# Optimization experiments

Measured on AMD Instinct MI355X. Metric: run time of the kernel, lower is better.

Reference implementation:

```python
import math
import jax, jax.numpy as jnp
import numpy as np

B, S, D, H, L, V = 2, 1024, 1024, 16, 6, 256
HD = D // H  # 64
PAD = 0


def setup_inputs() -> dict:
    key = jax.random.key(0)
    ks = jax.random.split(key, 22)
    s = 0.02
    f32 = jnp.float32
    inp = {
        "x": jax.random.randint(ks[0], (B, S), 0, V, dtype=jnp.int32),
        "emb": (jax.random.normal(ks[1], (V, D)) * s).astype(f32),
        "Wq": (jax.random.normal(ks[2], (L, D, D)) * s).astype(f32),
        "bq": jnp.zeros((L, D), f32),
        "Wk": (jax.random.normal(ks[3], (L, D, D)) * s).astype(f32),
        "bk": jnp.zeros((L, D), f32),
        "Wv": (jax.random.normal(ks[4], (L, D, D)) * s).astype(f32),
        "bv": jnp.zeros((L, D), f32),
        "Wo": (jax.random.normal(ks[5], (L, D, D)) * s).astype(f32),
        "bo": jnp.zeros((L, D), f32),
        "W1": (jax.random.normal(ks[6], (L, D, D // 2)) * s).astype(f32),
        "b1": jnp.zeros((L, D // 2), f32),
        "W2": (jax.random.normal(ks[7], (L, D // 2, D)) * s).astype(f32),
        "b2": jnp.zeros((L, D), f32),
        "g1": jnp.ones((L, D), f32),
        "be1": jnp.zeros((L, D), f32),
        "g2": jnp.ones((L, D), f32),
        "be2": jnp.zeros((L, D), f32),
        "E": jax.random.normal(ks[8], (L, S, HD)).astype(f32),  # relative pos embeddings, non-trainable
        "Wf": (jax.random.normal(ks[9], (D, V)) * s).astype(f32),
        "bf": jnp.zeros((V,), f32),
    }
    return inp


def _layernorm(x, g, b, eps=1e-6):
    mu = jnp.mean(x, axis=-1, keepdims=True)
    var = jnp.mean((x - mu) ** 2, axis=-1, keepdims=True)
    return (x - mu) * jax.lax.rsqrt(var + eps) * g + b


def _pos_encoding():
    # embed[p, i] = sin(p * exp(-ln(1e4)*i/D) * exp(ln(1e4)*(i%2)/D) + 0.5*pi*(i%2))
    i = jnp.arange(D, dtype=jnp.float32)
    par = jnp.mod(i, 2.0)
    rate = jnp.exp(-math.log(10000.0) * i / D) * jnp.exp(math.log(10000.0) * par / D)
    pos = jnp.arange(S, dtype=jnp.float32)
    return jnp.sin(pos[:, None] * rate[None, :] + 0.5 * math.pi * par[None, :])  # [S, D]


def _skew(QE):
    # Music Transformer skewing: pad one col on the left, reshape, drop first row.
    padded = jnp.pad(QE, ((0, 0), (0, 0), (0, 0), (1, 0)))  # [B,H,S,S+1]
    reshaped = padded.reshape(B, H, S + 1, S)
    return reshaped[:, :, 1:, :]  # [B,H,S,S]


def reference(x, emb, Wq, bq, Wk, bk, Wv, bv, Wo, bo, W1, b1, W2, b2,
              g1, be1, g2, be2, E, Wf, bf):
    pe = _pos_encoding()
    # look-ahead mask: pad positions OR strictly-future positions
    pad_mask = (x == PAD)[:, None, None, :]                      # [B,1,1,S]
    causal = jnp.triu(jnp.ones((S, S), bool), k=1)[None, None]   # [1,1,S,S]
    neg = (pad_mask | causal).astype(jnp.float32) * -1e9         # [B,1,S,S]
    # QE mask: keep qe[i, j] only where j >= S-1-i (upper-right triangle)
    idx = jnp.arange(S)
    qe_mask = (idx[None, :] >= (S - 1 - idx)[:, None]).astype(jnp.float32)

    h = emb[x] * math.sqrt(D) + pe[None]  # [B,S,D]
    scale = 1.0 / math.sqrt(HD)
    for l in range(L):
        q = (h @ Wq[l] + bq[l]).reshape(B, S, H, HD).transpose(0, 2, 1, 3)
        k = (h @ Wk[l] + bk[l]).reshape(B, S, H, HD).transpose(0, 2, 1, 3)
        v = (h @ Wv[l] + bv[l]).reshape(B, S, H, HD).transpose(0, 2, 1, 3)
        QE = jnp.einsum('bhld,md->bhlm', q, E[l]) * qe_mask
        Srel = _skew(QE)
        logits = (jnp.einsum('bhld,bhmd->bhlm', q, k) + Srel) * scale + neg
        aw = jax.nn.softmax(logits, axis=-1)
        attn = jnp.einsum('bhlm,bhmd->bhld', aw, v)
        attn = attn.transpose(0, 2, 1, 3).reshape(B, S, D)
        ao = attn @ Wo[l] + bo[l]
        o1 = _layernorm(ao, g1[l], be1[l])          # NOTE: no residual, as in source
        f = jax.nn.relu(o1 @ W1[l] + b1[l]) @ W2[l] + b2[l]
        h = _layernorm(f, g2[l], be2[l])
    return h @ Wf + bf  # [B,S,V]
```

## Files before the change

### kernel.cpp

```cpp
#include <hip/hip_runtime.h>
#include <hip/hip_bf16.h>


typedef __attribute__((ext_vector_type(8))) short  s8_t;
typedef __attribute__((ext_vector_type(4))) short  s4_t;
typedef __attribute__((ext_vector_type(8))) __bf16 bf8_t;
typedef __attribute__((ext_vector_type(4))) float  f4v;

static __device__ __forceinline__ short f2bf(float f) {
  union { float f; unsigned u; } a; a.f = f;
  unsigned u = a.u;
  u += 0x7fffu + ((u >> 16) & 1u);
  return (short)(u >> 16);
}
static __device__ __forceinline__ float bf2f(short s) {
  union { float f; unsigned u; } a;
  a.u = ((unsigned)(unsigned short)s) << 16;
  return a.f;
}
static __device__ __forceinline__ f4v mfma16(s8_t a, s8_t b, f4v c) {
  return __builtin_amdgcn_mfma_f32_16x16x32_bf16(
      __builtin_bit_cast(bf8_t, a), __builtin_bit_cast(bf8_t, b), c, 0, 0, 0);
}
static __device__ __forceinline__ void gld16(const short* g, short* l) {
  __builtin_amdgcn_global_load_lds(
      (const __attribute__((address_space(1))) void*)g,
      (__attribute__((address_space(3))) void*)l, 16, 0, 0);
}

static __device__ const int IT_TAB[40] = {
  15,15,15,15, 14,14,14,14, 13,13,13,13, 12,12,12,12,
  11,11,11, 10,10,10, 9,9,9, 8,8,8,
  7,7, 6,6, 5,5, 4,4, 3, 2, 1, 0};
static __device__ const int CW_TAB[40] = {
  0,1,2,3, 0,1,2,3, 0,1,2,3, 0,1,2,3,
  0,1,2, 0,1,2, 0,1,2, 0,1,2,
  0,1, 0,1, 0,1, 0,1, 0, 0, 0, 0};

__global__ void prep_weights(
    const float* __restrict__ Wq, const float* __restrict__ Wk,
    const float* __restrict__ Wv, const float* __restrict__ Wo,
    const float* __restrict__ W1, const float* __restrict__ W2,
    const float* __restrict__ Wf,
    short* __restrict__ qkvT, short* __restrict__ WoT, short* __restrict__ W1T,
    short* __restrict__ W2T, short* __restrict__ WfT) {
  __shared__ float tile[32][33];
  int z = blockIdx.x;
  const float* in; short* out; int R, C; long outBS; int rowOff = 0;
  if (z < 18432) {
    R = 1024; C = 1024; outBS = (long)3072 * 1024; out = qkvT;
    if (z < 6144)       { in = Wq; }
    else if (z < 12288) { in = Wk; rowOff = 1024; z -= 6144; }
    else                { in = Wv; rowOff = 2048; z -= 12288; }
  } else if (z < 24576) { in = Wo; out = WoT; R = 1024; C = 1024; outBS = (long)1024 * 1024; z -= 18432; }
  else if (z < 27648)   { in = W1; out = W1T; R = 1024; C = 512;  outBS = (long)512 * 1024;  z -= 24576; }
  else if (z < 30720)   { in = W2; out = W2T; R = 512;  C = 1024; outBS = (long)1024 * 512;  z -= 27648; }
  else                  { in = Wf; out = WfT; R = 1024; C = 256;  outBS = 0;                 z -= 30720; }
  const int nx = C >> 5, ny = R >> 5;
  const int per = nx * ny;
  const int l = z / per, rem = z % per;
  const int cx = rem % nx, cy = rem / nx;
  in += (long)l * R * C;
  out += (long)l * outBS + (long)rowOff * R;
  const int c0 = cx * 32, r0 = cy * 32;
  const int tx = threadIdx.x, ty = threadIdx.y;
#pragma unroll
  for (int i = 0; i < 4; i++)
    tile[ty + i * 8][tx] = in[(long)(r0 + ty + i * 8) * C + c0 + tx];
  __syncthreads();
#pragma unroll
  for (int i = 0; i < 4; i++)
    out[(long)(c0 + ty + i * 8) * R + r0 + tx] = f2bf(tile[tx][ty + i * 8]);
}

__global__ __launch_bounds__(256) void prep_misc(
    const int* __restrict__ x, const float* __restrict__ emb,
    const float* __restrict__ E,
    const float* __restrict__ bq, const float* __restrict__ bk,
    const float* __restrict__ bv,
    short* __restrict__ h, short* __restrict__ Ebf,
    float* __restrict__ qkvB, int* __restrict__ fnp) {
  const int z = blockIdx.x;
  const int tid = threadIdx.x;
  if (z < 2048) {
    const int s = z & 1023;
    const int xv = x[z];
    const int c = tid << 2;
    const float4 e = *(const float4*)(emb + (long)xv * 1024 + c);
    const float ev[4] = {e.x, e.y, e.z, e.w};
    s4_t o;
#pragma unroll
    for (int i = 0; i < 4; i++) {
      const int d = c + i;
      const float par = (float)(d & 1);
      const float rate = expf(-9.210340371976184f * (float)d / 1024.0f) *
                         expf(9.210340371976184f * par / 1024.0f);
      const float pe = sinf((float)s * rate + 1.5707963267948966f * par);
      o[i] = f2bf(ev[i] * 32.0f + pe);
    }
    *(s4_t*)(h + (long)z * 1024 + c) = o;
  } else if (z < 2432) {
    const long i = ((long)(z - 2048) * 256 + tid) * 4;
    const float4 t = *(const float4*)(E + i);
    s4_t o = {f2bf(t.x), f2bf(t.y), f2bf(t.z), f2bf(t.w)};
    *(s4_t*)(Ebf + i) = o;
  } else if (z < 2504) {
    const int idx = (z - 2432) * 256 + tid;
    const int l = idx / 3072, n = idx % 3072;
    float v = (n < 1024) ? bq[l * 1024 + n]
            : (n < 2048) ? bk[l * 1024 + n - 1024]
                         : bv[l * 1024 + n - 2048];
    qkvB[idx] = v;
  } else {
    if (tid < 64) {
      const int b = z - 2504;
      int first = 1024;
      for (int j0 = 0; j0 < 1024; j0 += 64) {
        unsigned long long m = __ballot(x[b * 1024 + j0 + tid] != 0);
        if (m) { first = j0 + __ffsll(m) - 1; break; }
      }
      if (tid == 0) fnp[b] = first;
    }
  }
}

__global__ __launch_bounds__(256) void ln_kernel(const short* __restrict__ in,
                                                 short* __restrict__ out,
                                                 const float* __restrict__ g,
                                                 const float* __restrict__ be) {
  __shared__ float red[4];
  __shared__ float red2[4];
  const int row = blockIdx.x;
  const int tid = threadIdx.x;
  const int c = tid << 2;
  const s4_t xv = *(const s4_t*)(in + (long)row * 1024 + c);
  const float x0 = bf2f(xv[0]), x1 = bf2f(xv[1]), x2 = bf2f(xv[2]), x3 = bf2f(xv[3]);
  float s = x0 + x1 + x2 + x3;
#pragma unroll
  for (int off = 1; off < 64; off <<= 1) s += __shfl_xor(s, off);
  const int wave = tid >> 6, lane = tid & 63;
  if (lane == 0) red[wave] = s;
  __syncthreads();
  const float mu = (red[0] + red[1] + red[2] + red[3]) * (1.0f / 1024.0f);
  const float d0 = x0 - mu, d1 = x1 - mu, d2 = x2 - mu, d3 = x3 - mu;
  float q = d0 * d0 + d1 * d1 + d2 * d2 + d3 * d3;
#pragma unroll
  for (int off = 1; off < 64; off <<= 1) q += __shfl_xor(q, off);
  if (lane == 0) red2[wave] = q;
  __syncthreads();
  const float var = (red2[0] + red2[1] + red2[2] + red2[3]) * (1.0f / 1024.0f);
  const float rs = rsqrtf(var + 1e-6f);
  const float4 gv = *(const float4*)(g + c);
  const float4 bv = *(const float4*)(be + c);
  s4_t o = {f2bf(d0 * rs * gv.x + bv.x), f2bf(d1 * rs * gv.y + bv.y),
            f2bf(d2 * rs * gv.z + bv.z), f2bf(d3 * rs * gv.w + bv.w)};
  *(s4_t*)(out + (long)row * 1024 + c) = o;
}

template <int BM, int BN, int WR, int WC, int OUT_BF16, int RELU>
__global__ __launch_bounds__(256) void gemm_lds(
    const short* __restrict__ A, const short* __restrict__ BT,
    void* __restrict__ Cv, const float* __restrict__ biasp,
    int K, int lda, int ldb, int ldc) {
  constexpr int AR = BM / 64, BR = BN / 64;
  constexpr int FI = BM / WR / 16, FJ = BN / WC / 16;
  __shared__ short As[BM * 32];
  __shared__ short Bs[BN * 32];
  const int bm = blockIdx.y * BM, bn = blockIdx.x * BN;
  const int tid = threadIdx.x;
  const int wave = tid >> 6, lane = tid & 63;
  const int quad = lane >> 4, l16 = lane & 15;
  const int wr = wave / WC, wc = wave % WC;
  const int wm = wr * (BM / WR), wn = wc * (BN / WC);

  const short* Ag = A + (long)(bm + wave * 16 + (lane >> 2)) * lda + ((lane & 3) << 3);
  const short* Bg = BT + (long)(bn + wave * 16 + (lane >> 2)) * ldb + ((lane & 3) << 3);

  f4v acc[FI][FJ];
#pragma unroll
  for (int i = 0; i < FI; i++)
#pragma unroll
    for (int j = 0; j < FJ; j++) {
      f4v zz = {0.f, 0.f, 0.f, 0.f};
      acc[i][j] = zz;
    }

  for (int k0 = 0; k0 < K; k0 += 32) {
#pragma unroll
    for (int r = 0; r < AR; r++)
      gld16(Ag + (long)r * 64 * lda + k0, As + r * 2048 + wave * 512);
#pragma unroll
    for (int r = 0; r < BR; r++)
      gld16(Bg + (long)r * 64 * ldb + k0, Bs + r * 2048 + wave * 512);
    __syncthreads();
    s8_t af[FI], bfr[FJ];
#pragma unroll
    for (int t = 0; t < FI; t++)
      af[t] = *(const s8_t*)&As[(wm + t * 16 + l16) * 32 + quad * 8];
#pragma unroll
    for (int t = 0; t < FJ; t++)
      bfr[t] = *(const s8_t*)&Bs[(wn + t * 16 + l16) * 32 + quad * 8];
#pragma unroll
    for (int ti = 0; ti < FI; ti++)
#pragma unroll
      for (int tj = 0; tj < FJ; tj++)
        acc[ti][tj] = mfma16(af[ti], bfr[tj], acc[ti][tj]);
    __syncthreads();
  }

#pragma unroll
  for (int ti = 0; ti < FI; ti++) {
#pragma unroll
    for (int tj = 0; tj < FJ; tj++) {
      const int n = bn + wn + tj * 16 + l16;
      const float bval = biasp ? biasp[n] : 0.f;
#pragma unroll
      for (int r = 0; r < 4; r++) {
        const int m = bm + wm + ti * 16 + quad * 4 + r;
        float vv = acc[ti][tj][r] + bval;
        if (RELU) vv = fmaxf(vv, 0.f);
        if (OUT_BF16) ((short*)Cv)[(long)m * ldc + n] = f2bf(vv);
        else          ((float*)Cv)[(long)m * ldc + n] = vv;
      }
    }
  }
}

__global__ __launch_bounds__(256) void attn_main(
    const short* __restrict__ qkv, const short* __restrict__ Eb,
    const int* __restrict__ xids, const int* __restrict__ fnp,
    float* __restrict__ PO, float* __restrict__ PM, float* __restrict__ PL,
    short* __restrict__ outb) {
  __shared__ short Ks2[8][128][8];
  __shared__ short Vt[64][136];
  __shared__ short Gs[4][16][152];
  __shared__ float kneg[128];

  const int bh = blockIdx.x, b = bh >> 4, hh = bh & 15;
  const int yy = blockIdx.y;
  const bool fbp = (yy >= 40);
  const int itile = fbp ? (yy - 40) : IT_TAB[yy];
  const int cw = fbp ? 0 : CW_TAB[yy];
  const int fb = fnp[b];
  const int i0g = itile * 64;
  if (fbp && fb <= i0g) return;

  const int tid = threadIdx.x;
  const int wave = tid >> 6, lane = tid & 63, quad = lane >> 4, l16 = lane & 15;
  const int i0 = i0g + wave * 16;

  s8_t aq[2];
  {
    const short* qp = qkv + ((long)(b * 1024 + i0 + l16)) * 3072 + hh * 64 + quad * 8;
    aq[0] = *(const s8_t*)qp;
    aq[1] = *(const s8_t*)(qp + 32);
  }

  f4v o[4];
#pragma unroll
  for (int nt = 0; nt < 4; nt++) { f4v zz = {0.f, 0.f, 0.f, 0.f}; o[nt] = zz; }
  float m_run[4] = {-INFINITY, -INFINITY, -INFINITY, -INFINITY};
  float l_run[4] = {0.f, 0.f, 0.f, 0.f};

  const int half = wave >> 1;
  const int krow = ((wave & 1) << 6) + lane;
  const short* kbase = qkv + (long)b * 1024 * 3072 + 1024 + hh * 64 + wave * 8;
  const short* vbase = qkv + (long)b * 1024 * 3072 + 2048 + hh * 64 + half * 32;
  short* gs = &Gs[wave][0][0];

  const int jBeg = fbp ? 0 : cw * 256;
  const int jEnd = fbp ? 1024 : min(cw * 256 + 256, i0g + 64);

  for (int j0 = jBeg; j0 < jEnd; j0 += 128) {
    {
      const long k1 = min(j0 + lane, 1023);
      const long k2 = min(j0 + 64 + lane, 1023);
      gld16(kbase + k1 * 3072, &Ks2[wave][0][0]);
      gld16(kbase + k2 * 3072, &Ks2[wave][64][0]);
      gld16(kbase + k1 * 3072 + 32, &Ks2[wave + 4][0][0]);
      gld16(kbase + k2 * 3072 + 32, &Ks2[wave + 4][64][0]);
      const long kv = min(j0 + krow, 1023);
      const short* vrow = vbase + kv * 3072;
      const s8_t v0 = *(const s8_t*)(vrow);
      const s8_t v1 = *(const s8_t*)(vrow + 8);
      const s8_t v2 = *(const s8_t*)(vrow + 16);
      const s8_t v3 = *(const s8_t*)(vrow + 24);
#pragma unroll
      for (int t = 0; t < 8; t++) {
        Vt[half * 32 + t][krow] = v0[t];
        Vt[half * 32 + 8 + t][krow] = v1[t];
        Vt[half * 32 + 16 + t][krow] = v2[t];
        Vt[half * 32 + 24 + t][krow] = v3[t];
      }
    }
    if (tid < 128) kneg[tid] = (xids[b * 1024 + min(j0 + tid, 1023)] == 0) ? -1e9f : 0.0f;

    {
      const int mW = 1008 - i0g - wave * 16 + j0;
#pragma unroll
      for (int t = 0; t < 9; t++) {
        const int m = min(mW + t * 16 + l16, 1023);
        const short* ep = Eb + m * 64 + quad * 8;
        const s8_t eb0 = *(const s8_t*)ep;
        const s8_t eb1 = *(const s8_t*)(ep + 32);
        f4v g = {0.f, 0.f, 0.f, 0.f};
        g = mfma16(aq[0], eb0, g);
        g = mfma16(aq[1], eb1, g);
#pragma unroll
        for (int r = 0; r < 4; r++)
          gs[(quad * 4 + r) * 152 + t * 16 + l16] = f2bf(g[r]);
      }
    }
    __syncthreads();

    float p[8][4];
    const int irow = i0 + quad * 4;
#pragma unroll
    for (int jt = 0; jt < 8; jt++) {
      const s8_t k0f = *(const s8_t*)&Ks2[quad][jt * 16 + l16][0];
      const s8_t k1f = *(const s8_t*)&Ks2[4 + quad][jt * 16 + l16][0];
      f4v zz = {0.f, 0.f, 0.f, 0.f};
      zz = mfma16(aq[0], k0f, zz);
      zz = mfma16(aq[1], k1f, zz);
      const int j = j0 + jt * 16 + l16;
      const float kn = kneg[jt * 16 + l16];
#pragma unroll
      for (int r = 0; r < 4; r++) {
        const int rr = quad * 4 + r;
        const float smv = bf2f(gs[rr * 151 + 15 + jt * 16 + l16]);
        const bool causal = (j <= irow + r);
        const float srel = causal ? smv : 0.f;
        const float kk = fbp ? 0.f : (causal ? kn : -1e9f);
        p[jt][r] = (zz[r] + srel) * 0.125f + kk;
      }
    }

    float alpha[4];
#pragma unroll
    for (int r = 0; r < 4; r++) {
      float mx = p[0][r];
#pragma unroll
      for (int jt = 1; jt < 8; jt++) mx = fmaxf(mx, p[jt][r]);
      mx = fmaxf(mx, __shfl_xor(mx, 1));
      mx = fmaxf(mx, __shfl_xor(mx, 2));
      mx = fmaxf(mx, __shfl_xor(mx, 4));
      mx = fmaxf(mx, __shfl_xor(mx, 8));
      const float mnew = fmaxf(m_run[r], mx);
      alpha[r] = expf(m_run[r] - mnew);
      float ps = 0.f;
#pragma unroll
      for (int jt = 0; jt < 8; jt++) {
        p[jt][r] = expf(p[jt][r] - mnew);
        ps += p[jt][r];
      }
      ps += __shfl_xor(ps, 1);
      ps += __shfl_xor(ps, 2);
      ps += __shfl_xor(ps, 4);
      ps += __shfl_xor(ps, 8);
      l_run[r] = l_run[r] * alpha[r] + ps;
      m_run[r] = mnew;
    }

#pragma unroll
    for (int jt = 0; jt < 8; jt++)
#pragma unroll
      for (int r = 0; r < 4; r++)
        gs[(quad * 4 + r) * 152 + jt * 16 + l16] = f2bf(p[jt][r]);
#pragma unroll
    for (int nt = 0; nt < 4; nt++)
#pragma unroll
      for (int r = 0; r < 4; r++)
        o[nt][r] *= alpha[r];

#pragma unroll
    for (int ks4 = 0; ks4 < 4; ks4++) {
      const s8_t ap = *(const s8_t*)&gs[l16 * 152 + ks4 * 32 + quad * 8];
#pragma unroll
      for (int nt = 0; nt < 4; nt++) {
        const s8_t vf = *(const s8_t*)&Vt[nt * 16 + l16][ks4 * 32 + quad * 8];
        o[nt] = mfma16(ap, vf, o[nt]);
      }
    }
    __syncthreads();
  }

  if (fbp) {
#pragma unroll
    for (int nt = 0; nt < 4; nt++)
#pragma unroll
      for (int r = 0; r < 4; r++) {
        const int i = i0 + quad * 4 + r;
        if (i < fb)
          outb[((long)(b * 1024 + i)) * 1024 + hh * 64 + nt * 16 + l16] =
              f2bf(o[nt][r] / l_run[r]);
      }
  } else if (yy >= 36) {
#pragma unroll
    for (int nt = 0; nt < 4; nt++)
#pragma unroll
      for (int r = 0; r < 4; r++) {
        const int i = i0 + quad * 4 + r;
        if (i >= fb)
          outb[((long)(b * 1024 + i)) * 1024 + hh * 64 + nt * 16 + l16] =
              f2bf(o[nt][r] / l_run[r]);
      }
  } else {
    const long part = (long)(bh * 16 + itile) * 4 + cw;
    float* po = PO + part * 4096;
#pragma unroll
    for (int nt = 0; nt < 4; nt++)
#pragma unroll
      for (int r = 0; r < 4; r++) {
        const int row = wave * 16 + quad * 4 + r;
        po[row * 64 + nt * 16 + l16] = o[nt][r];
      }
    if (l16 == 0) {
#pragma unroll
      for (int r = 0; r < 4; r++) {
        const int row = wave * 16 + quad * 4 + r;
        PM[part * 64 + row] = m_run[r];
        PL[part * 64 + row] = l_run[r];
      }
    }
  }
}

__global__ __launch_bounds__(256) void attn_combine(
    const float* __restrict__ PO, const float* __restrict__ PM,
    const float* __restrict__ PL, const int* __restrict__ fnp,
    short* __restrict__ outb) {
  const int id = blockIdx.x;
  const int bh = id / 12, itile = 4 + id % 12;
  const int b = bh >> 4, hh = bh & 15;
  const int nc = (itile >> 2) + 1;
  const int row = threadIdx.x >> 2, seg = (threadIdx.x & 3) << 4;
  const long base = (long)(bh * 16 + itile) * 4;
  const int i = itile * 64 + row;
  if (i < fnp[b]) return;

  float mv[4];
  float M = -INFINITY;
  for (int c = 0; c < nc; c++) {
    mv[c] = PM[(base + c) * 64 + row];
    M = fmaxf(M, mv[c]);
  }
  f4v acc[4];
#pragma unroll
  for (int t = 0; t < 4; t++) { f4v zz = {0.f, 0.f, 0.f, 0.f}; acc[t] = zz; }
  float l = 0.f;
  for (int c = 0; c < nc; c++) {
    const float w = expf(mv[c] - M);
    l += w * PL[(base + c) * 64 + row];
    const float* po = PO + (base + c) * 4096 + row * 64 + seg;
#pragma unroll
    for (int t = 0; t < 4; t++) {
      const f4v v = *(const f4v*)(po + t * 4);
      acc[t] += w * v;
    }
  }
  const float inv = 1.0f / l;
  short* op = outb + ((long)(b * 1024 + i)) * 1024 + hh * 64 + seg;
#pragma unroll
  for (int t = 0; t < 4; t++) {
    s4_t o = {f2bf(acc[t][0] * inv), f2bf(acc[t][1] * inv),
              f2bf(acc[t][2] * inv), f2bf(acc[t][3] * inv)};
    *(s4_t*)(op + t * 4) = o;
  }
}

extern "C" void kernel_launch(void* const* d_in, const int* in_sizes, int n_in,
                              void* d_out, int out_size, void* d_ws, size_t ws_size,
                              hipStream_t stream) {
  const int*   x   = (const int*)d_in[0];
  const float* emb = (const float*)d_in[1];
  const float* Wq  = (const float*)d_in[2];
  const float* bq  = (const float*)d_in[3];
  const float* Wk  = (const float*)d_in[4];
  const float* bk  = (const float*)d_in[5];
  const float* Wv  = (const float*)d_in[6];
  const float* bv  = (const float*)d_in[7];
  const float* Wo  = (const float*)d_in[8];
  const float* bo  = (const float*)d_in[9];
  const float* W1  = (const float*)d_in[10];
  const float* b1  = (const float*)d_in[11];
  const float* W2  = (const float*)d_in[12];
  const float* b2  = (const float*)d_in[13];
  const float* g1  = (const float*)d_in[14];
  const float* be1 = (const float*)d_in[15];
  const float* g2  = (const float*)d_in[16];
  const float* be2 = (const float*)d_in[17];
  const float* E   = (const float*)d_in[18];
  const float* Wf  = (const float*)d_in[19];
  const float* bfv = (const float*)d_in[20];

  char* p = (char*)d_ws;
  auto alloc = [&](size_t bytes) {
    char* r = p;
    p += (bytes + 255) & ~(size_t)255;
    return r;
  };
  short* h    = (short*)alloc(2048ull * 1024 * 2);
  short* qkv  = (short*)alloc(2048ull * 3072 * 2);
  short* attn = (short*)alloc(2048ull * 1024 * 2);
  short* tmp  = (short*)alloc(2048ull * 1024 * 2);
  short* mid  = (short*)alloc(2048ull * 512 * 2);
  short* qkvT = (short*)alloc(6ull * 3072 * 1024 * 2);
  short* WoT  = (short*)alloc(6ull * 1024 * 1024 * 2);
  short* W1T  = (short*)alloc(6ull * 512 * 1024 * 2);
  short* W2T  = (short*)alloc(6ull * 1024 * 512 * 2);
  short* WfT  = (short*)alloc(256ull * 1024 * 2);
  short* Ebf  = (short*)alloc(6ull * 1024 * 64 * 2);
  float* qkvB = (float*)alloc(6ull * 3072 * 4);
  int*   fnp  = (int*)alloc(256);
  float* PO   = (float*)alloc(2048ull * 4096 * 4);
  float* PM   = (float*)alloc(2048ull * 64 * 4);
  float* PL   = (float*)alloc(2048ull * 64 * 4);

  prep_weights<<<30976, dim3(32, 8), 0, stream>>>(
      Wq, Wk, Wv, Wo, W1, W2, Wf, qkvT, WoT, W1T, W2T, WfT);
  prep_misc<<<2506, 256, 0, stream>>>(x, emb, E, bq, bk, bv, h, Ebf, qkvB, fnp);

  for (int l = 0; l < 6; l++) {
    const long wOff = (long)l * 1024 * 1024;
    const long w12Off = (long)l * 512 * 1024;
    gemm_lds<128, 128, 2, 2, 1, 0><<<dim3(24, 16), 256, 0, stream>>>(
        h, qkvT + (long)l * 3072 * 1024, qkv, qkvB + l * 3072, 1024, 1024, 1024, 3072);
    attn_main<<<dim3(32, 56), 256, 0, stream>>>(
        qkv, Ebf + (long)l * 1024 * 64, x, fnp, PO, PM, PL, attn);
    attn_combine<<<384, 256, 0, stream>>>(PO, PM, PL, fnp, attn);
    gemm_lds<64, 64, 2, 2, 1, 0><<<dim3(16, 32), 256, 0, stream>>>(
        attn, WoT + wOff, tmp, bo + l * 1024, 1024, 1024, 1024, 1024);
    ln_kernel<<<2048, 256, 0, stream>>>(tmp, tmp, g1 + l * 1024, be1 + l * 1024);
    gemm_lds<64, 64, 2, 2, 1, 1><<<dim3(8, 32), 256, 0, stream>>>(
        tmp, W1T + w12Off, mid, b1 + l * 512, 1024, 1024, 1024, 512);
    gemm_lds<64, 64, 2, 2, 1, 0><<<dim3(16, 32), 256, 0, stream>>>(
        mid, W2T + w12Off, h, b2 + l * 1024, 512, 512, 512, 1024);
    ln_kernel<<<2048, 256, 0, stream>>>(h, h, g2 + l * 1024, be2 + l * 1024);
  }
  gemm_lds<64, 64, 2, 2, 0, 0><<<dim3(4, 32), 256, 0, stream>>>(
      h, WfT, (float*)d_out, bfv, 1024, 1024, 1024, 256);
}
```

Measured before the change: 979.0 us.

## Skip fully-masked causal tiles in attention, use fast exp, enlarge GEMM tiles

The attention main loop now works out, per 128-key block, how many 16-column subtiles lie inside the causal window. It skips QK^T MFMAs, relative-position MFMAs, exps and PV MFMAs for the subtiles beyond that point, and zero-fills the probability subtiles that the PV pass still reads. Blocks that lie fully below the diagonal take a branch with no mask logic. expf is replaced by __expf in the softmax and combine kernels. The Wo and W2 GEMMs switch to 128x64 tiles, which halves their grid. The runtime jtEnd checks inside unrolled loops add branches and may raise register pressure, and __expf gives slightly lower precision.

After: 1.050 ms. +7.3%, slower.

```diff
diff --git a/kernel.cpp b/kernel.cpp
--- a/kernel.cpp
+++ b/kernel.cpp
@@ -272,6 +272,10 @@
   const int jEnd = fbp ? 1024 : min(cw * 256 + 256, i0g + 64);
 
   for (int j0 = jBeg; j0 < jEnd; j0 += 128) {
+    const int jtEnd = fbp ? 8 : min(8, ((i0 + 15 - j0) >> 4) + 1);
+    const int ks4End = (jtEnd + 1) >> 1;
+    const bool fullc = !fbp && (j0 + 127 <= i0);
+
     {
       const long k1 = min(j0 + lane, 1023);
       const long k2 = min(j0 + 64 + lane, 1023);
@@ -299,6 +303,7 @@
       const int mW = 1008 - i0g - wave * 16 + j0;
 #pragma unroll
       for (int t = 0; t < 9; t++) {
+        if (t > jtEnd) continue;
         const int m = min(mW + t * 16 + l16, 1023);
         const short* ep = Eb + m * 64 + quad * 8;
         const s8_t eb0 = *(const s8_t*)ep;
@@ -317,6 +322,7 @@
     const int irow = i0 + quad * 4;
 #pragma unroll
     for (int jt = 0; jt < 8; jt++) {
+      if (jt >= jtEnd) continue;
       const s8_t k0f = *(const s8_t*)&Ks2[quad][jt * 16 + l16][0];
       const s8_t k1f = *(const s8_t*)&Ks2[4 + quad][jt * 16 + l16][0];
       f4v zz = {0.f, 0.f, 0.f, 0.f};
@@ -324,14 +330,23 @@
       zz = mfma16(aq[1], k1f, zz);
       const int j = j0 + jt * 16 + l16;
       const float kn = kneg[jt * 16 + l16];
-#pragma unroll
-      for (int r = 0; r < 4; r++) {
-        const int rr = quad * 4 + r;
-        const float smv = bf2f(gs[rr * 151 + 15 + jt * 16 + l16]);
-        const bool causal = (j <= irow + r);
-        const float srel = causal ? smv : 0.f;
-        const float kk = fbp ? 0.f : (causal ? kn : -1e9f);
-        p[jt][r] = (zz[r] + srel) * 0.125f + kk;
+      if (fullc) {
+#pragma unroll
+        for (int r = 0; r < 4; r++) {
+          const int rr = quad * 4 + r;
+          const float smv = bf2f(gs[rr * 151 + 15 + jt * 16 + l16]);
+          p[jt][r] = (zz[r] + smv) * 0.125f + kn;
+        }
+      } else {
+#pragma unroll
+        for (int r = 0; r < 4; r++) {
+          const int rr = quad * 4 + r;
+          const float smv = bf2f(gs[rr * 151 + 15 + jt * 16 + l16]);
+          const bool causal = (j <= irow + r);
+          const float srel = causal ? smv : 0.f;
+          const float kk = fbp ? 0.f : (causal ? kn : -1e9f);
+          p[jt][r] = (zz[r] + srel) * 0.125f + kk;
+        }
       }
     }
 
@@ -340,17 +355,19 @@
     for (int r = 0; r < 4; r++) {
       float mx = p[0][r];
 #pragma unroll
-      for (int jt = 1; jt < 8; jt++) mx = fmaxf(mx, p[jt][r]);
+      for (int jt = 1; jt < 8; jt++)
+        if (jt < jtEnd) mx = fmaxf(mx, p[jt][r]);
       mx = fmaxf(mx, __shfl_xor(mx, 1));
       mx = fmaxf(mx, __shfl_xor(mx, 2));
       mx = fmaxf(mx, __shfl_xor(mx, 4));
       mx = fmaxf(mx, __shfl_xor(mx, 8));
       const float mnew = fmaxf(m_run[r], mx);
-      alpha[r] = expf(m_run[r] - mnew);
+      alpha[r] = __expf(m_run[r] - mnew);
       float ps = 0.f;
 #pragma unroll
       for (int jt = 0; jt < 8; jt++) {
-        p[jt][r] = expf(p[jt][r] - mnew);
+        if (jt >= jtEnd) continue;
+        p[jt][r] = __expf(p[jt][r] - mnew);
         ps += p[jt][r];
       }
       ps += __shfl_xor(ps, 1);
@@ -362,10 +379,17 @@
     }
 
 #pragma unroll
-    for (int jt = 0; jt < 8; jt++)
-#pragma unroll
-      for (int r = 0; r < 4; r++)
-        gs[(quad * 4 + r) * 152 + jt * 16 + l16] = f2bf(p[jt][r]);
+    for (int jt = 0; jt < 8; jt++) {
+      if (jt < jtEnd) {
+#pragma unroll
+        for (int r = 0; r < 4; r++)
+          gs[(quad * 4 + r) * 152 + jt * 16 + l16] = f2bf(p[jt][r]);
+      } else if (jt < 2 * ks4End) {
+#pragma unroll
+        for (int r = 0; r < 4; r++)
+          gs[(quad * 4 + r) * 152 + jt * 16 + l16] = 0;
+      }
+    }
 #pragma unroll
     for (int nt = 0; nt < 4; nt++)
 #pragma unroll
@@ -374,6 +398,7 @@
 
 #pragma unroll
     for (int ks4 = 0; ks4 < 4; ks4++) {
+      if (ks4 >= ks4End) continue;
       const s8_t ap = *(const s8_t*)&gs[l16 * 152 + ks4 * 32 + quad * 8];
 #pragma unroll
       for (int nt = 0; nt < 4; nt++) {
@@ -449,7 +474,7 @@
   for (int t = 0; t < 4; t++) { f4v zz = {0.f, 0.f, 0.f, 0.f}; acc[t] = zz; }
   float l = 0.f;
   for (int c = 0; c < nc; c++) {
-    const float w = expf(mv[c] - M);
+    const float w = __expf(mv[c] - M);
     l += w * PL[(base + c) * 64 + row];
     const float* po = PO + (base + c) * 4096 + row * 64 + seg;
 #pragma unroll
@@ -528,12 +553,12 @@
     attn_main<<<dim3(32, 56), 256, 0, stream>>>(
         qkv, Ebf + (long)l * 1024 * 64, x, fnp, PO, PM, PL, attn);
     attn_combine<<<384, 256, 0, stream>>>(PO, PM, PL, fnp, attn);
-    gemm_lds<64, 64, 2, 2, 1, 0><<<dim3(16, 32), 256, 0, stream>>>(
+    gemm_lds<128, 64, 2, 2, 1, 0><<<dim3(16, 16), 256, 0, stream>>>(
         attn, WoT + wOff, tmp, bo + l * 1024, 1024, 1024, 1024, 1024);
     ln_kernel<<<2048, 256, 0, stream>>>(tmp, tmp, g1 + l * 1024, be1 + l * 1024);
     gemm_lds<64, 64, 2, 2, 1, 1><<<dim3(8, 32), 256, 0, stream>>>(
         tmp, W1T + w12Off, mid, b1 + l * 512, 1024, 1024, 1024, 512);
-    gemm_lds<64, 64, 2, 2, 1, 0><<<dim3(16, 32), 256, 0, stream>>>(
+    gemm_lds<128, 64, 2, 2, 1, 0><<<dim3(16, 16), 256, 0, stream>>>(
         mid, W2T + w12Off, h, b2 + l * 1024, 512, 512, 512, 1024);
     ln_kernel<<<2048, 256, 0, stream>>>(h, h, g2 + l * 1024, be2 + l * 1024);
   }
```
